# Performance work log

Measured on AMD Instinct MI355X. Metric: run time of the kernel, lower is better.

The kernel has to match this reference:

```python
import jax, jax.numpy as jnp
import numpy as np

DIST = 200.0
BBOX_SP = 24
N_COARSE = 64
N_BOXES = 10
SAMPLES_ALL = N_COARSE + 2 * N_BOXES  # 84
FR_POS = 10
FR_DIR = 4
NSEM = 50
WID = 256
MERGES = [(39, 41), (27, 26), (28, 26), (29, 26), (30, 26), (31, 26), (9, 8), (35, 13)]


def posenc(x, L):
    f = 2.0 ** jnp.arange(L, dtype=x.dtype)
    xb = x[..., None, :] * f[:, None]                      # [..., L, 3]
    enc = jnp.concatenate([jnp.sin(xb), jnp.cos(xb)], -1)  # [..., L, 6]
    return jnp.concatenate([x, enc.reshape(x.shape[:-1] + (-1,))], -1)


def sample_pdf(bins, weights, n):
    # deterministic inverse-CDF sampling (det=True), bins [B,N,M], weights [B,N,M-1]
    pdf = weights / jnp.sum(weights, -1, keepdims=True)
    cdf = jnp.cumsum(pdf, -1)
    cdf = jnp.concatenate([jnp.zeros_like(cdf[..., :1]), cdf], -1)   # [B,N,M]
    B, N, M = cdf.shape
    u = jnp.linspace(0.0, 1.0, n, dtype=bins.dtype)
    cdf_f = cdf.reshape(B * N, M)
    bins_f = bins.reshape(B * N, M)
    u_f = jnp.broadcast_to(u, (B * N, n))
    inds = jax.vmap(lambda c, uu: jnp.searchsorted(c, uu, side='right'))(cdf_f, u_f)
    below = jnp.clip(inds - 1, 0, M - 1)
    above = jnp.clip(inds, 0, M - 1)
    cdf_b = jnp.take_along_axis(cdf_f, below, 1)
    cdf_a = jnp.take_along_axis(cdf_f, above, 1)
    bin_b = jnp.take_along_axis(bins_f, below, 1)
    bin_a = jnp.take_along_axis(bins_f, above, 1)
    denom = jnp.where(cdf_a - cdf_b < 1e-5, 1.0, cdf_a - cdf_b)
    t = (u_f - cdf_b) / denom
    return (bin_b + t * (bin_a - bin_b)).reshape(B, N, n)


def setup_inputs() -> dict:
    key = jax.random.key(0)
    ks = jax.random.split(key, 16)
    B, N = 1, 2048
    rays_o = jax.random.normal(ks[0], (B, N, 3)) * 2.0
    rays_d = jax.random.normal(ks[1], (B, N, 3))
    rays = jnp.concatenate([rays_o, rays_d], -1)
    near = jax.random.uniform(ks[2], (B, N, N_BOXES), minval=5.0, maxval=150.0)
    far = near + jax.random.uniform(ks[3], (B, N, N_BOXES), minval=5.0, maxval=60.0)
    inst = jax.random.randint(ks[4], (B, N, N_BOXES), 0, 20).astype(jnp.float32)
    label = jax.random.randint(ks[5], (B, N, N_BOXES), 1, NSEM).astype(jnp.float32)
    intersection = jnp.stack([near, far, inst, label], -1)  # [B,N,10,4]
    bg_noise = jax.random.uniform(ks[6], (B, N, SAMPLES_ALL))

    def lin(k, fi, fo):
        return jax.random.normal(k, (fi, fo)) / np.sqrt(fi)

    d_x = 3 + 6 * FR_POS  # 63
    d_d = 3 + 6 * FR_DIR  # 27
    params = dict(
        w_in=lin(ks[7], d_x, WID), b_in=jnp.zeros((WID,)),
        w_h=jax.random.normal(ks[8], (6, WID, WID)) / np.sqrt(WID), b_h=jnp.zeros((6, WID)),
        w_skip=lin(ks[9], WID + d_x, WID), b_skip=jnp.zeros((WID,)),
        w_sigma=lin(ks[10], WID, 1), b_sigma=jnp.zeros((1,)),
        w_feat=lin(ks[11], WID, WID), b_feat=jnp.zeros((WID,)),
        w_rgb1=lin(ks[12], WID + d_d, 128), b_rgb1=jnp.zeros((128,)),
        w_rgb2=lin(ks[13], 128, 3), b_rgb2=jnp.zeros((3,)),
        w_sem=lin(ks[14], WID, NSEM), b_sem=jnp.zeros((NSEM,)),
    )
    out = {'rays': rays, 'intersection': intersection, 'bg_noise': bg_noise}
    out.update(params)
    return out


def reference(rays, intersection, bg_noise, w_in, b_in, w_h, b_h, w_skip, b_skip,
              w_sigma, b_sigma, w_feat, b_feat, w_rgb1, b_rgb1, w_rgb2, b_rgb2,
              w_sem, b_sem):
    B, N, _ = rays.shape
    rays_o, rays_d = rays[..., :3], rays[..., 3:6]
    scale = jnp.linalg.norm(rays_d, axis=-1)  # [B,N]

    # --- ray sampling inside boxes + uniform-PDF resampling ---
    near, far = intersection[..., 0], intersection[..., 1]  # [B,N,10]
    t = jnp.linspace(0.0, 1.0, BBOX_SP)
    z_box = near[..., None] + (far - near)[..., None] * t       # [B,N,10,24]
    z_bound = jnp.concatenate([z_box[..., 0] - 1e-5, z_box[..., -1] + 1e-5], axis=2)  # [B,N,20]
    zf = jnp.sort(z_box.reshape(B, N, -1), axis=2)              # [B,N,240]
    z = sample_pdf(zf, jnp.ones_like(zf[..., 1:]), N_COARSE)    # [B,N,64]
    z = jnp.concatenate([z, z_bound], axis=2)                   # [B,N,84]
    z = jnp.where(z < 0.0, DIST + 20.0 * bg_noise, z)
    z = jnp.sort(z, axis=2)

    # --- NeRF MLP on sample points ---
    xyz = (rays_o[:, :, None] + rays_d[:, :, None] * z[..., None] / scale[..., None, None]) / DIST
    dirs = rays_d / scale[..., None]
    x_enc = posenc(xyz, FR_POS)                                 # [B,N,S,63]
    h = jax.nn.relu(x_enc @ w_in + b_in)
    for i in range(3):
        h = jax.nn.relu(h @ w_h[i] + b_h[i])
    h = jax.nn.relu(jnp.concatenate([h, x_enc], -1) @ w_skip + b_skip)
    for i in range(3, 6):
        h = jax.nn.relu(h @ w_h[i] + b_h[i])
    sigma = (h @ w_sigma + b_sigma)[..., 0]                     # [B,N,S]
    sem = h @ w_sem + b_sem                                     # [B,N,S,50]
    feat = h @ w_feat + b_feat
    d_enc = posenc(dirs, FR_DIR)                                # [B,N,27]
    d_enc = jnp.broadcast_to(d_enc[:, :, None, :], feat.shape[:-1] + (d_enc.shape[-1],))
    hr = jax.nn.relu(jnp.concatenate([feat, d_enc], -1) @ w_rgb1 + b_rgb1)
    rgb = hr @ w_rgb2 + b_rgb2                                  # [B,N,S,3]

    # --- semantic one-hot scatter + boundary masks (no-grad region) ---
    zs = jax.lax.stop_gradient(z)
    nearb = intersection[:, :, None, :, 0]                      # [B,N,1,10]
    farb = intersection[:, :, None, :, 1]
    inside = (zs[..., None] > nearb) & (zs[..., None] < farb)   # [B,N,S,10]
    d1 = zs[..., None] - farb
    d2 = nearb - zs[..., None]
    mask_bound = jnp.any(((d1 > 0) & (d1 < 1e-3)) | ((d2 > 0) & (d2 < 1e-3)), axis=-1)
    labels = intersection[..., 3].astype(jnp.int32)             # [B,N,10]
    oh_box = jax.nn.one_hot(labels, NSEM)                       # [B,N,10,50]
    one_hot = jnp.max(inside[..., None].astype(jnp.float32) * oh_box[:, :, None, :, :], axis=3)
    s0 = one_hot.sum(-1)
    mask_bbox = (zs < DIST) & (s0 == 0.0)
    mask_bg = (zs > DIST) & (s0 == 0.0)
    one_hot = one_hot.at[..., 0].set(jnp.where(mask_bbox, 1.0, one_hot[..., 0]))
    one_hot = one_hot.at[..., 23].set(jnp.where(mask_bg, 1.0, one_hot[..., 23]))
    for src, dst in MERGES:  # training-mode class merging (box/car/park/gate)
        one_hot = one_hot.at[..., dst].set(jnp.maximum(one_hot[..., dst], one_hot[..., src]))
        one_hot = one_hot.at[..., src].set(0.0)
    one_hot = jax.lax.stop_gradient(one_hot)

    # zero density outside boxes and at box boundaries
    sigma = jnp.where(mask_bbox | mask_bound, 0.0, sigma)

    # --- volumetric compositing (raw2outputs_semantic_joint) ---
    z_true = z / scale[..., None]
    dists = jnp.concatenate([z_true[..., 1:] - z_true[..., :-1],
                             jnp.full_like(z_true[..., :1], 1e10)], -1) * scale[..., None]
    alpha = 1.0 - jnp.exp(-jax.nn.relu(sigma) * dists)
    trans = jnp.cumprod(jnp.concatenate([jnp.ones_like(alpha[..., :1]),
                                         1.0 - alpha + 1e-10], -1)[..., :-1], -1)
    w = alpha * trans                                           # [B,N,S]
    rgb_map = jnp.einsum('bns,bnsc->bnc', w, jax.nn.sigmoid(rgb))
    depth = jnp.sum(w * z_true, -1)
    acc = jnp.sum(w, -1)
    sem_map = jnp.einsum('bns,bnsc->bnc', w, sem)
    return jnp.concatenate([rgb_map, depth[..., None], acc[..., None], sem_map], -1)  # [B,N,55]
```

## Files before the change

### kernel.cpp

```cpp
#include <hip/hip_runtime.h>

typedef _Float16 half8 __attribute__((ext_vector_type(8)));
typedef float f32x4  __attribute__((ext_vector_type(4)));
typedef float f32x16 __attribute__((ext_vector_type(16)));

#define NRAYS 2048
#define SAMP 84
#define NPTS (NRAYS*SAMP)
#define SEMSTR 52

#define WT0_OFF   0
#define WTH_OFF   16384
#define WTS_OFF   409600
#define WTHD_OFF  491520
#define WTR1_OFF  573440
#define WTR2_OFF  610304
#define WT_TOTAL  614400
#define NBIAS     2512

#define OFF_WT    ((size_t)0)
#define OFF_BIAS  ((size_t)1228800)
#define OFF_Z     (OFF_BIAS + (size_t)NBIAS*4)
#define OFF_SCALE (OFF_Z + (size_t)NPTS*4)
#define OFF_SIGMA (OFF_SCALE + (size_t)NRAYS*4)
#define OFF_RGB   (OFF_SIGMA + (size_t)NPTS*4)
#define OFF_SEM   (OFF_RGB + (size_t)NPTS*12)

__global__ __launch_bounds__(256) void prep_kernel(
    const float* __restrict__ w_in,  const float* __restrict__ w_h,
    const float* __restrict__ w_skip,const float* __restrict__ w_sigma,
    const float* __restrict__ w_feat,const float* __restrict__ w_rgb1,
    const float* __restrict__ w_rgb2,const float* __restrict__ w_sem,
    const float* __restrict__ b_in,  const float* __restrict__ b_h,
    const float* __restrict__ b_skip,const float* __restrict__ b_sigma,
    const float* __restrict__ b_feat,const float* __restrict__ b_rgb1,
    const float* __restrict__ b_rgb2,const float* __restrict__ b_sem,
    _Float16* __restrict__ wt, float* __restrict__ bias)
{
  int idx = blockIdx.x*256 + threadIdx.x;
  if (idx < WT_TOTAL) {
    float v; int n, k, l, h, kt, F, rem;
    if (idx < WTH_OFF) {
      F = idx >> 11; rem = idx & 2047; kt = rem >> 9; int q = rem & 511;
      l = q >> 3; h = q & 7;
      n = F*32 + (l&31); k = kt*16 + ((l>>5)<<3) + h;
      v = (k < 63) ? w_in[k*256 + n] : 0.f;
    } else if (idx < WTS_OFF) {
      int r = idx - WTH_OFF; int i = r >> 16; int rr = r & 65535;
      F = rr >> 13; rem = rr & 8191; kt = rem >> 9; int q = rem & 511;
      l = q >> 3; h = q & 7;
      n = F*32 + (l&31); k = kt*16 + ((l>>5)<<3) + h;
      v = w_h[(i<<16) + (k<<8) + n];
    } else if (idx < WTHD_OFF) {
      int r = idx - WTS_OFF;
      F = r / 10240; rem = r % 10240; kt = rem >> 9; int q = rem & 511;
      l = q >> 3; h = q & 7;
      n = F*32 + (l&31); k = kt*16 + ((l>>5)<<3) + h;
      v = (k < 319) ? w_skip[k*256 + n] : 0.f;
    } else if (idx < WTR1_OFF) {
      int r = idx - WTHD_OFF;
      F = r >> 13; rem = r & 8191; kt = rem >> 9; int q = rem & 511;
      l = q >> 3; h = q & 7;
      n = F*32 + (l&31); k = kt*16 + ((l>>5)<<3) + h;
      v = (n < 256) ? w_feat[(k<<8) + n]
        : (n < 306) ? w_sem[k*50 + (n-256)]
        : (n == 306)? w_sigma[k] : 0.f;
    } else if (idx < WTR2_OFF) {
      int r = idx - WTR1_OFF;
      F = r / 9216; rem = r % 9216; kt = rem >> 9; int q = rem & 511;
      l = q >> 3; h = q & 7;
      n = F*32 + (l&31); k = kt*16 + ((l>>5)<<3) + h;
      v = (k < 283) ? w_rgb1[k*128 + n] : 0.f;
    } else {
      int r = idx - WTR2_OFF;
      kt = r >> 9; int q = r & 511;
      l = q >> 3; h = q & 7;
      n = (l&31); k = kt*16 + ((l>>5)<<3) + h;
      v = (n < 3) ? w_rgb2[k*3 + n] : 0.f;
    }
    wt[idx] = (_Float16)v;
  } else if (idx < WT_TOTAL + NBIAS) {
    int j = idx - WT_TOTAL; float v;
    if (j < 2048) {
      int i = j >> 8, c = j & 255;
      v = (i==0) ? b_in[c] : (i<4) ? b_h[(i-1)*256+c]
        : (i==4) ? b_skip[c] : b_h[(i-2)*256+c];
    } else if (j < 2368) {
      int c = j - 2048;
      v = (c<256) ? b_feat[c] : (c<306) ? b_sem[c-256]
        : (c==306) ? b_sigma[0] : 0.f;
    } else if (j < 2496) v = b_rgb1[j-2368];
    else { int c = j-2496; v = (c<3) ? b_rgb2[c] : 0.f; }
    bias[j] = v;
  }
}

__global__ __launch_bounds__(256) void sample_kernel(
    const float* __restrict__ rays, const float* __restrict__ inter,
    const float* __restrict__ noise, float* __restrict__ zbuf,
    float* __restrict__ scaleb)
{
  __shared__ float sv[240], ss[240], z2[84];
  const int ray = blockIdx.x, t = threadIdx.x;
  const float* bx = inter + (size_t)ray*40;
  if (t < 240) {
    int b = t/24, j = t%24;
    float nr = bx[b*4], fr = bx[b*4+1];
    float tj = (j==23) ? 1.f : (float)j * (1.f/23.f);
    sv[t] = nr + (fr-nr)*tj;
  }
  __syncthreads();
  if (t < 240) {
    float v = sv[t]; int r = 0;
    for (int i = 0; i < 240; ++i) { float vi = sv[i]; r += (vi < v) || (vi == v && i < t); }
    ss[r] = v;
  }
  __syncthreads();
  if (t < 64) {
    float z;
    if (t == 63) z = ss[239];
    else { int num = t*239; int k = num/63; float f = (float)(num - k*63)*(1.f/63.f);
           z = ss[k] + f*(ss[k+1]-ss[k]); }
    z2[t] = z;
  } else if (t < 84) {
    int b = t - 64;
    z2[t] = (b < 10) ? (bx[b*4] - 1e-5f) : (bx[(b-10)*4+1] + 1e-5f);
  }
  __syncthreads();
  if (t < 84) { float z = z2[t]; if (z < 0.f) z = 200.f + 20.f*noise[(size_t)ray*84 + t]; z2[t] = z; }
  __syncthreads();
  if (t < 84) {
    float v = z2[t]; int r = 0;
    for (int i = 0; i < 84; ++i) { float vi = z2[i]; r += (vi < v) || (vi == v && i < t); }
    zbuf[(size_t)ray*84 + r] = v;
  }
  if (t == 0) {
    float dx = rays[ray*6+3], dy = rays[ray*6+4], dz = rays[ray*6+5];
    scaleb[ray] = sqrtf(dx*dx + dy*dy + dz*dz);
  }
}

#define LDS_TOTAL 40960

__device__ __forceinline__ uint32_t laddr(int m, int k) {
  return (uint32_t)(m*640) + (uint32_t)((((k>>3)^(m&7))<<4) + ((k&7)<<1));
}
struct __attribute__((aligned(8))) H4 { _Float16 h[4]; };

__device__ __forceinline__ float xenc_val(int j, float x0, float x1, float x2) {
  if (j >= 63) return 0.f;
  if (j < 3) return j==0?x0:(j==1?x1:x2);
  int q = j-3, lf = q/6, r = q%6, ci = r%3;
  float xc = (ci==0)?x0:((ci==1)?x1:x2);
  float arg = xc * (float)(1<<lf);
  return (r<3) ? sinf(arg) : cosf(arg);
}
__device__ __forceinline__ float denc_val(int c, float u0, float u1, float u2) {
  if (c >= 27) return 0.f;
  if (c < 3) return c==0?u0:(c==1?u1:u2);
  int q = c-3, lf = q/6, r = q%6, ci = r%3;
  float uc = (ci==0)?u0:((ci==1)?u1:u2);
  float arg = uc * (float)(1<<lf);
  return (r<3) ? sinf(arg) : cosf(arg);
}

template<int KT, int NF, int MODE, bool RELU, int XOFF, bool INPLACE>
__device__ __forceinline__ void gemm(uint8_t* smem,
    const _Float16* __restrict__ WT, int fbase, const float* __restrict__ bias0,
    int p0, float* __restrict__ sigmaws, _Float16* __restrict__ semws)
{
  constexpr int MF = 2;
  const int t = threadIdx.x;
  const int l = t & 63, wn = t >> 6;
  const int lr = l & 31, lg = l >> 5;
  constexpr int DW   = (KT <= 3) ? KT : 4;
  constexpr int LEAD = (KT <= 3) ? KT : 3;
  f32x16 acc[NF][MF];
#pragma unroll
  for (int i = 0; i < NF; ++i)
#pragma unroll
    for (int j = 0; j < MF; ++j)
#pragma unroll
      for (int r = 0; r < 16; ++r) acc[i][j][r] = 0.f;
  const _Float16* wb = WT + (size_t)((fbase + wn*NF)*KT)*512 + (size_t)l*8;
  half8 av[DW][NF];
  half8 bv[2][MF];
  auto baddr = [&](int mf, int kt)->uint32_t {
    return laddr(mf*32 + lr, XOFF + kt*16 + lg*8);
  };
#pragma unroll
  for (int d = 0; d < LEAD && d < KT; ++d)
#pragma unroll
    for (int nf = 0; nf < NF; ++nf)
      av[d][nf] = *(const half8*)(wb + (size_t)(nf*KT + d)*512);
#pragma unroll
  for (int mf = 0; mf < MF; ++mf)
    bv[0][mf] = *(const half8*)(smem + baddr(mf, 0));
#pragma unroll
  for (int kt = 0; kt < KT; ++kt) {
    if (kt + 1 < KT) {
#pragma unroll
      for (int mf = 0; mf < MF; ++mf)
        bv[(kt+1)&1][mf] = *(const half8*)(smem + baddr(mf, kt+1));
    }
    if (kt + LEAD < KT) {
#pragma unroll
      for (int nf = 0; nf < NF; ++nf)
        av[(kt+LEAD)%DW][nf] = *(const half8*)(wb + (size_t)(nf*KT + kt + LEAD)*512);
    }
    __builtin_amdgcn_sched_barrier(0);
#pragma unroll
    for (int nf = 0; nf < NF; ++nf)
#pragma unroll
      for (int mf = 0; mf < MF; ++mf)
        acc[nf][mf] = __builtin_amdgcn_mfma_f32_32x32x16_f16(
            av[kt%DW][nf], bv[kt&1][mf], acc[nf][mf], 0, 0, 0);
    __builtin_amdgcn_sched_barrier(0);
  }
  if (INPLACE) __syncthreads();
#pragma unroll
  for (int nf = 0; nf < NF; ++nf) {
    const int ncol0 = (fbase + wn*NF + nf)*32;
#pragma unroll
    for (int mf = 0; mf < MF; ++mf) {
      const int m = mf*32 + lr;
      const f32x16 v = acc[nf][mf];
#pragma unroll
      for (int g = 0; g < 4; ++g) {
        const int nst = ncol0 + 8*g + 4*lg;
        const f32x4 b4 = *(const f32x4*)(bias0 + nst);
        float x0 = v[4*g+0] + b4[0], x1 = v[4*g+1] + b4[1];
        float x2 = v[4*g+2] + b4[2], x3 = v[4*g+3] + b4[3];
        if (RELU) { x0 = fmaxf(x0,0.f); x1 = fmaxf(x1,0.f);
                    x2 = fmaxf(x2,0.f); x3 = fmaxf(x3,0.f); }
        if (MODE == 0) {
          H4 hh; hh.h[0]=(_Float16)x0; hh.h[1]=(_Float16)x1;
                 hh.h[2]=(_Float16)x2; hh.h[3]=(_Float16)x3;
          *(H4*)(smem + laddr(m, nst)) = hh;
        } else {
          const int cb = nst - 256;
          const int pp = p0 + m;
          if (cb <= 44) {
            H4 hh; hh.h[0]=(_Float16)x0; hh.h[1]=(_Float16)x1;
                   hh.h[2]=(_Float16)x2; hh.h[3]=(_Float16)x3;
            *(H4*)(semws + (size_t)pp*SEMSTR + cb) = hh;
          } else if (cb == 48) {
            semws[(size_t)pp*SEMSTR + 48] = (_Float16)x0;
            semws[(size_t)pp*SEMSTR + 49] = (_Float16)x1;
            sigmaws[pp] = x2;
          }
        }
      }
    }
  }
}

__device__ __forceinline__ void gemm_rgb2(uint8_t* smem,
    const _Float16* __restrict__ WT, const float* __restrict__ bias,
    int p0, float* __restrict__ rgbws)
{
  const int t = threadIdx.x;
  const int l = t & 63, w = t >> 6;
  if (w >= 2) return;
  const int lr = l & 31, lg = l >> 5;
  f32x16 acc;
#pragma unroll
  for (int r = 0; r < 16; ++r) acc[r] = 0.f;
  const _Float16* wb = WT + (size_t)l*8;
#pragma unroll
  for (int kt = 0; kt < 8; ++kt) {
    half8 a = *(const half8*)(wb + (size_t)kt*512);
    half8 b = *(const half8*)(smem + laddr(w*32 + lr, kt*16 + lg*8));
    acc = __builtin_amdgcn_mfma_f32_32x32x16_f16(a, b, acc, 0, 0, 0);
  }
  if (lg == 0) {
    const int pp = p0 + w*32 + lr;
#pragma unroll
    for (int r = 0; r < 3; ++r)
      rgbws[(size_t)pp*3 + r] = acc[r] + bias[r];
  }
}

__global__ __launch_bounds__(256,3) void mlp_kernel(
    const float* __restrict__ rays, const float* __restrict__ zbuf,
    const float* __restrict__ scaleb, const _Float16* __restrict__ wt,
    const float* __restrict__ bias, float* __restrict__ sigmaws,
    float* __restrict__ rgbws, _Float16* __restrict__ semws)
{
  extern __shared__ uint8_t smem[];
  const int p0 = blockIdx.x*64;
  const int t = threadIdx.x;
  const int m = t & 63, g = t >> 6;
  const int p = p0 + m;
  const int ray = p / SAMP;
  const float sc = scaleb[ray];
  const float z  = zbuf[p];
  const float ox = rays[ray*6+0], oy = rays[ray*6+1], oz = rays[ray*6+2];
  const float dx = rays[ray*6+3], dy = rays[ray*6+4], dz = rays[ray*6+5];
  const float x0 = (ox + dx*z/sc)/200.f;
  const float x1 = (oy + dy*z/sc)/200.f;
  const float x2 = (oz + dz*z/sc)/200.f;
  const float u0 = dx/sc, u1 = dy/sc, u2 = dz/sc;
  {
    union { _Float16 hv[8]; half8 v; } u8;
#pragma unroll
    for (int hf = 0; hf < 2; ++hf) {
      const int j0 = g*16 + hf*8;
#pragma unroll
      for (int jj = 0; jj < 8; ++jj) u8.hv[jj] = (_Float16)xenc_val(j0+jj, x0, x1, x2);
      *(half8*)(smem + laddr(m, 256 + j0)) = u8.v;
    }
  }
  __syncthreads();
  gemm<4 ,2,0,true ,256,false>(smem, wt+WT0_OFF,         0, bias+0,    p0, sigmaws, semws); __syncthreads();
  gemm<16,2,0,true ,0  ,true >(smem, wt+WTH_OFF+0*65536, 0, bias+256,  p0, sigmaws, semws); __syncthreads();
  gemm<16,2,0,true ,0  ,true >(smem, wt+WTH_OFF+1*65536, 0, bias+512,  p0, sigmaws, semws); __syncthreads();
  gemm<16,2,0,true ,0  ,true >(smem, wt+WTH_OFF+2*65536, 0, bias+768,  p0, sigmaws, semws); __syncthreads();
  gemm<20,2,0,true ,0  ,true >(smem, wt+WTS_OFF,         0, bias+1024, p0, sigmaws, semws);
  {
    union { _Float16 hv[8]; half8 v; } u8;
    const int c0 = g*8;
#pragma unroll
    for (int cc = 0; cc < 8; ++cc) u8.hv[cc] = (_Float16)denc_val(c0+cc, u0, u1, u2);
    *(half8*)(smem + laddr(m, 256 + c0)) = u8.v;
  }
  __syncthreads();
  gemm<16,2,0,true ,0  ,true >(smem, wt+WTH_OFF+3*65536, 0, bias+1280, p0, sigmaws, semws); __syncthreads();
  gemm<16,2,0,true ,0  ,true >(smem, wt+WTH_OFF+4*65536, 0, bias+1536, p0, sigmaws, semws); __syncthreads();
  gemm<16,2,0,true ,0  ,true >(smem, wt+WTH_OFF+5*65536, 0, bias+1792, p0, sigmaws, semws); __syncthreads();
  if ((t >> 6) < 2)
    gemm<16,1,1,false,0 ,false>(smem, wt+WTHD_OFF,        8, bias+2048, p0, sigmaws, semws);
  gemm<16,2,0,false,0  ,true >(smem, wt+WTHD_OFF,        0, bias+2048, p0, sigmaws, semws); __syncthreads();
  gemm<18,1,0,true ,0  ,true >(smem, wt+WTR1_OFF,        0, bias+2368, p0, sigmaws, semws); __syncthreads();
  gemm_rgb2(smem, wt+WTR2_OFF, bias+2496, p0, rgbws);
}

__global__ __launch_bounds__(128) void comp_kernel(
    const float* __restrict__ inter, const float* __restrict__ zbuf,
    const float* __restrict__ scaleb, const float* __restrict__ sigmaws,
    const float* __restrict__ rgbws, const _Float16* __restrict__ semws,
    float* __restrict__ out)
{
  __shared__ float zt[84], alpha[84], wgt[84];
  const int ray = blockIdx.x, t = threadIdx.x;
  const float sc = scaleb[ray];
  const float* bx = inter + (size_t)ray*40;
  if (t < 84) zt[t] = zbuf[(size_t)ray*84 + t] / sc;
  __syncthreads();
  if (t < 84) {
    const float z = zbuf[(size_t)ray*84 + t];
    bool inside = false, bound = false;
    for (int b = 0; b < 10; ++b) {
      const float nr = bx[b*4], fr = bx[b*4+1];
      inside = inside || (z > nr && z < fr);
      const float d1 = z - fr, d2 = nr - z;
      bound = bound || (d1 > 0.f && d1 < 1e-3f) || (d2 > 0.f && d2 < 1e-3f);
    }
    float sg = sigmaws[(size_t)ray*84 + t];
    const bool bbox = (z < 200.f) && !inside;
    if (bbox || bound) sg = 0.f;
    sg = fmaxf(sg, 0.f);
    const float dist = (t < 83) ? (zt[t+1] - zt[t])*sc : 1e10f*sc;
    alpha[t] = 1.f - expf(-sg*dist);
  }
  __syncthreads();
  if (t == 0) {
    float T = 1.f;
    for (int s = 0; s < 84; ++s) { wgt[s] = alpha[s]*T; T *= (1.f - alpha[s] + 1e-10f); }
  }
  __syncthreads();
  if (t < 55) {
    float a = 0.f;
    const size_t base = (size_t)ray*84;
    if (t < 50) {
      for (int s = 0; s < 84; ++s) a += wgt[s]*(float)semws[(base+s)*SEMSTR + t];
      out[(size_t)ray*55 + 5 + t] = a;
    } else if (t < 53) {
      const int c = t - 50;
      for (int s = 0; s < 84; ++s) { const float r = rgbws[(base+s)*3 + c]; a += wgt[s]/(1.f + expf(-r)); }
      out[(size_t)ray*55 + c] = a;
    } else if (t == 53) {
      for (int s = 0; s < 84; ++s) a += wgt[s]*zt[s];
      out[(size_t)ray*55 + 3] = a;
    } else {
      for (int s = 0; s < 84; ++s) a += wgt[s];
      out[(size_t)ray*55 + 4] = a;
    }
  }
}

extern "C" void kernel_launch(void* const* d_in, const int* in_sizes, int n_in,
                              void* d_out, int out_size, void* d_ws, size_t ws_size,
                              hipStream_t stream) {
  const float* rays   = (const float*)d_in[0];
  const float* inter  = (const float*)d_in[1];
  const float* noise  = (const float*)d_in[2];
  const float* w_in   = (const float*)d_in[3];
  const float* b_in   = (const float*)d_in[4];
  const float* w_h    = (const float*)d_in[5];
  const float* b_h    = (const float*)d_in[6];
  const float* w_skip = (const float*)d_in[7];
  const float* b_skip = (const float*)d_in[8];
  const float* w_sig  = (const float*)d_in[9];
  const float* b_sig  = (const float*)d_in[10];
  const float* w_feat = (const float*)d_in[11];
  const float* b_feat = (const float*)d_in[12];
  const float* w_rgb1 = (const float*)d_in[13];
  const float* b_rgb1 = (const float*)d_in[14];
  const float* w_rgb2 = (const float*)d_in[15];
  const float* b_rgb2 = (const float*)d_in[16];
  const float* w_sem  = (const float*)d_in[17];
  const float* b_sem  = (const float*)d_in[18];

  uint8_t* ws = (uint8_t*)d_ws;
  _Float16* wt    = (_Float16*)(ws + OFF_WT);
  float* bias     = (float*)(ws + OFF_BIAS);
  float* zbuf     = (float*)(ws + OFF_Z);
  float* scaleb   = (float*)(ws + OFF_SCALE);
  float* sigmaws  = (float*)(ws + OFF_SIGMA);
  float* rgbws    = (float*)(ws + OFF_RGB);
  _Float16* semws = (_Float16*)(ws + OFF_SEM);

  prep_kernel<<<dim3((WT_TOTAL + NBIAS + 255)/256), dim3(256), 0, stream>>>(
      w_in, w_h, w_skip, w_sig, w_feat, w_rgb1, w_rgb2, w_sem,
      b_in, b_h, b_skip, b_sig, b_feat, b_rgb1, b_rgb2, b_sem, wt, bias);
  sample_kernel<<<dim3(NRAYS), dim3(256), 0, stream>>>(rays, inter, noise, zbuf, scaleb);
  mlp_kernel<<<dim3(NPTS/64), dim3(256), LDS_TOTAL, stream>>>(
      rays, zbuf, scaleb, wt, bias, sigmaws, rgbws, semws);
  comp_kernel<<<dim3(NRAYS), dim3(128), 0, stream>>>(
      inter, zbuf, scaleb, sigmaws, rgbws, semws, (float*)d_out);
}
```

Measured before the change: 292.6 us.

## Double MLP point tile per block and pack bias/ReLU epilogue in fp16

Each MLP block now handles 128 points instead of 64 (MF=4, LDS doubled, grid halved, occupancy hint lowered to 2). This reuses each loaded weight fragment across twice as many MFMAs. The hidden-layer epilogue now converts accumulators to packed fp16 first and does bias add and ReLU in half2, using a new fp16 bias buffer. The trade-offs are more registers and LDS per block, fewer resident blocks, and slightly lower epilogue precision. The early return for waves 2-3 in gemm_rgb2 was also removed, which may change which waves run that stage.

```diff
diff --git a/kernel.cpp b/kernel.cpp
--- a/kernel.cpp
+++ b/kernel.cpp
@@ -1,6 +1,7 @@
 #include <hip/hip_runtime.h>
 
 typedef _Float16 half8 __attribute__((ext_vector_type(8)));
+typedef __fp16  half2v __attribute__((ext_vector_type(2)));
 typedef float f32x4  __attribute__((ext_vector_type(4)));
 typedef float f32x16 __attribute__((ext_vector_type(16)));
 
@@ -20,7 +21,8 @@
 
 #define OFF_WT    ((size_t)0)
 #define OFF_BIAS  ((size_t)1228800)
-#define OFF_Z     (OFF_BIAS + (size_t)NBIAS*4)
+#define OFF_BIASH ((size_t)1238848)
+#define OFF_Z     ((size_t)1243904)
 #define OFF_SCALE (OFF_Z + (size_t)NPTS*4)
 #define OFF_SIGMA (OFF_SCALE + (size_t)NRAYS*4)
 #define OFF_RGB   (OFF_SIGMA + (size_t)NPTS*4)
@@ -35,7 +37,8 @@
     const float* __restrict__ b_skip,const float* __restrict__ b_sigma,
     const float* __restrict__ b_feat,const float* __restrict__ b_rgb1,
     const float* __restrict__ b_rgb2,const float* __restrict__ b_sem,
-    _Float16* __restrict__ wt, float* __restrict__ bias)
+    _Float16* __restrict__ wt, float* __restrict__ bias,
+    _Float16* __restrict__ biasH)
 {
   int idx = blockIdx.x*256 + threadIdx.x;
   if (idx < WT_TOTAL) {
@@ -92,6 +95,7 @@
     } else if (j < 2496) v = b_rgb1[j-2368];
     else { int c = j-2496; v = (c<3) ? b_rgb2[c] : 0.f; }
     bias[j] = v;
+    biasH[j] = (_Float16)v;
   }
 }
 
@@ -140,7 +144,7 @@
   }
 }
 
-#define LDS_TOTAL 40960
+#define LDS_TOTAL 81920
 
 __device__ __forceinline__ uint32_t laddr(int m, int k) {
   return (uint32_t)(m*640) + (uint32_t)((((k>>3)^(m&7))<<4) + ((k&7)<<1));
@@ -166,10 +170,11 @@
 
 template<int KT, int NF, int MODE, bool RELU, int XOFF, bool INPLACE>
 __device__ __forceinline__ void gemm(uint8_t* smem,
-    const _Float16* __restrict__ WT, int fbase, const float* __restrict__ bias0,
+    const _Float16* __restrict__ WT, int fbase,
+    const float* __restrict__ bias0, const _Float16* __restrict__ biasH0,
     int p0, float* __restrict__ sigmaws, _Float16* __restrict__ semws)
 {
-  constexpr int MF = 2;
+  constexpr int MF = 4;
   const int t = threadIdx.x;
   const int l = t & 63, wn = t >> 6;
   const int lr = l & 31, lg = l >> 5;
@@ -228,26 +233,32 @@
 #pragma unroll
       for (int g = 0; g < 4; ++g) {
         const int nst = ncol0 + 8*g + 4*lg;
-        const f32x4 b4 = *(const f32x4*)(bias0 + nst);
-        float x0 = v[4*g+0] + b4[0], x1 = v[4*g+1] + b4[1];
-        float x2 = v[4*g+2] + b4[2], x3 = v[4*g+3] + b4[3];
-        if (RELU) { x0 = fmaxf(x0,0.f); x1 = fmaxf(x1,0.f);
-                    x2 = fmaxf(x2,0.f); x3 = fmaxf(x3,0.f); }
         if (MODE == 0) {
-          H4 hh; hh.h[0]=(_Float16)x0; hh.h[1]=(_Float16)x1;
-                 hh.h[2]=(_Float16)x2; hh.h[3]=(_Float16)x3;
+          half2v h0 = __builtin_amdgcn_cvt_pkrtz(v[4*g+0], v[4*g+1]);
+          half2v h1 = __builtin_amdgcn_cvt_pkrtz(v[4*g+2], v[4*g+3]);
+          const half2v* bh = (const half2v*)(biasH0 + nst);
+          h0 = h0 + bh[0];
+          h1 = h1 + bh[1];
+          if (RELU) {
+            h0 = __builtin_elementwise_max(h0, (half2v)(__fp16)0);
+            h1 = __builtin_elementwise_max(h1, (half2v)(__fp16)0);
+          }
+          H4 hh; *(half2v*)&hh.h[0] = h0; *(half2v*)&hh.h[2] = h1;
           *(H4*)(smem + laddr(m, nst)) = hh;
         } else {
+          const f32x4 b4 = *(const f32x4*)(bias0 + nst);
+          float y0 = v[4*g+0] + b4[0], y1 = v[4*g+1] + b4[1];
+          float y2 = v[4*g+2] + b4[2], y3 = v[4*g+3] + b4[3];
           const int cb = nst - 256;
           const int pp = p0 + m;
           if (cb <= 44) {
-            H4 hh; hh.h[0]=(_Float16)x0; hh.h[1]=(_Float16)x1;
-                   hh.h[2]=(_Float16)x2; hh.h[3]=(_Float16)x3;
+            H4 hh; hh.h[0]=(_Float16)y0; hh.h[1]=(_Float16)y1;
+                   hh.h[2]=(_Float16)y2; hh.h[3]=(_Float16)y3;
             *(H4*)(semws + (size_t)pp*SEMSTR + cb) = hh;
           } else if (cb == 48) {
-            semws[(size_t)pp*SEMSTR + 48] = (_Float16)x0;
-            semws[(size_t)pp*SEMSTR + 49] = (_Float16)x1;
-            sigmaws[pp] = x2;
+            semws[(size_t)pp*SEMSTR + 48] = (_Float16)y0;
+            semws[(size_t)pp*SEMSTR + 49] = (_Float16)y1;
+            sigmaws[pp] = y2;
           }
         }
       }
@@ -261,7 +272,6 @@
 {
   const int t = threadIdx.x;
   const int l = t & 63, w = t >> 6;
-  if (w >= 2) return;
   const int lr = l & 31, lg = l >> 5;
   f32x16 acc;
 #pragma unroll
@@ -281,16 +291,17 @@
   }
 }
 
-__global__ __launch_bounds__(256,3) void mlp_kernel(
+__global__ __launch_bounds__(256,2) void mlp_kernel(
     const float* __restrict__ rays, const float* __restrict__ zbuf,
     const float* __restrict__ scaleb, const _Float16* __restrict__ wt,
-    const float* __restrict__ bias, float* __restrict__ sigmaws,
-    float* __restrict__ rgbws, _Float16* __restrict__ semws)
+    const float* __restrict__ bias, const _Float16* __restrict__ biasH,
+    float* __restrict__ sigmaws, float* __restrict__ rgbws,
+    _Float16* __restrict__ semws)
 {
   extern __shared__ uint8_t smem[];
-  const int p0 = blockIdx.x*64;
+  const int p0 = blockIdx.x*128;
   const int t = threadIdx.x;
-  const int m = t & 63, g = t >> 6;
+  const int m = t & 127, g = t >> 7;
   const int p = p0 + m;
   const int ray = p / SAMP;
   const float sc = scaleb[ray];
@@ -304,34 +315,37 @@
   {
     union { _Float16 hv[8]; half8 v; } u8;
 #pragma unroll
-    for (int hf = 0; hf < 2; ++hf) {
-      const int j0 = g*16 + hf*8;
+    for (int q = 0; q < 4; ++q) {
+      const int j0 = g*32 + q*8;
 #pragma unroll
       for (int jj = 0; jj < 8; ++jj) u8.hv[jj] = (_Float16)xenc_val(j0+jj, x0, x1, x2);
       *(half8*)(smem + laddr(m, 256 + j0)) = u8.v;
     }
   }
   __syncthreads();
-  gemm<4 ,2,0,true ,256,false>(smem, wt+WT0_OFF,         0, bias+0,    p0, sigmaws, semws); __syncthreads();
-  gemm<16,2,0,true ,0  ,true >(smem, wt+WTH_OFF+0*65536, 0, bias+256,  p0, sigmaws, semws); __syncthreads();
-  gemm<16,2,0,true ,0  ,true >(smem, wt+WTH_OFF+1*65536, 0, bias+512,  p0, sigmaws, semws); __syncthreads();
-  gemm<16,2,0,true ,0  ,true >(smem, wt+WTH_OFF+2*65536, 0, bias+768,  p0, sigmaws, semws); __syncthreads();
-  gemm<20,2,0,true ,0  ,true >(smem, wt+WTS_OFF,         0, bias+1024, p0, sigmaws, semws);
+  gemm<4 ,2,0,true ,256,false>(smem, wt+WT0_OFF,         0, bias+0,    biasH+0,    p0, sigmaws, semws); __syncthreads();
+  gemm<16,2,0,true ,0  ,true >(smem, wt+WTH_OFF+0*65536, 0, bias+256,  biasH+256,  p0, sigmaws, semws); __syncthreads();
+  gemm<16,2,0,true ,0  ,true >(smem, wt+WTH_OFF+1*65536, 0, bias+512,  biasH+512,  p0, sigmaws, semws); __syncthreads();
+  gemm<16,2,0,true ,0  ,true >(smem, wt+WTH_OFF+2*65536, 0, bias+768,  biasH+768,  p0, sigmaws, semws); __syncthreads();
+  gemm<20,2,0,true ,0  ,true >(smem, wt+WTS_OFF,         0, bias+1024, biasH+1024, p0, sigmaws, semws);
   {
     union { _Float16 hv[8]; half8 v; } u8;
-    const int c0 = g*8;
-#pragma unroll
-    for (int cc = 0; cc < 8; ++cc) u8.hv[cc] = (_Float16)denc_val(c0+cc, u0, u1, u2);
-    *(half8*)(smem + laddr(m, 256 + c0)) = u8.v;
-  }
-  __syncthreads();
-  gemm<16,2,0,true ,0  ,true >(smem, wt+WTH_OFF+3*65536, 0, bias+1280, p0, sigmaws, semws); __syncthreads();
-  gemm<16,2,0,true ,0  ,true >(smem, wt+WTH_OFF+4*65536, 0, bias+1536, p0, sigmaws, semws); __syncthreads();
-  gemm<16,2,0,true ,0  ,true >(smem, wt+WTH_OFF+5*65536, 0, bias+1792, p0, sigmaws, semws); __syncthreads();
+#pragma unroll
+    for (int hf = 0; hf < 2; ++hf) {
+      const int c0 = g*16 + hf*8;
+#pragma unroll
+      for (int cc = 0; cc < 8; ++cc) u8.hv[cc] = (_Float16)denc_val(c0+cc, u0, u1, u2);
+      *(half8*)(smem + laddr(m, 256 + c0)) = u8.v;
+    }
+  }
+  __syncthreads();
+  gemm<16,2,0,true ,0  ,true >(smem, wt+WTH_OFF+3*65536, 0, bias+1280, biasH+1280, p0, sigmaws, semws); __syncthreads();
+  gemm<16,2,0,true ,0  ,true >(smem, wt+WTH_OFF+4*65536, 0, bias+1536, biasH+1536, p0, sigmaws, semws); __syncthreads();
+  gemm<16,2,0,true ,0  ,true >(smem, wt+WTH_OFF+5*65536, 0, bias+1792, biasH+1792, p0, sigmaws, semws); __syncthreads();
   if ((t >> 6) < 2)
-    gemm<16,1,1,false,0 ,false>(smem, wt+WTHD_OFF,        8, bias+2048, p0, sigmaws, semws);
-  gemm<16,2,0,false,0  ,true >(smem, wt+WTHD_OFF,        0, bias+2048, p0, sigmaws, semws); __syncthreads();
-  gemm<18,1,0,true ,0  ,true >(smem, wt+WTR1_OFF,        0, bias+2368, p0, sigmaws, semws); __syncthreads();
+    gemm<16,1,1,false,0 ,false>(smem, wt+WTHD_OFF,        8, bias+2048, biasH+2048, p0, sigmaws, semws);
+  gemm<16,2,0,false,0  ,true >(smem, wt+WTHD_OFF,        0, bias+2048, biasH+2048, p0, sigmaws, semws); __syncthreads();
+  gemm<18,1,0,true ,0  ,true >(smem, wt+WTR1_OFF,        0, bias+2368, biasH+2368, p0, sigmaws, semws); __syncthreads();
   gemm_rgb2(smem, wt+WTR2_OFF, bias+2496, p0, rgbws);
 }
 
@@ -415,6 +429,7 @@
   uint8_t* ws = (uint8_t*)d_ws;
   _Float16* wt    = (_Float16*)(ws + OFF_WT);
   float* bias     = (float*)(ws + OFF_BIAS);
+  _Float16* biasH = (_Float16*)(ws + OFF_BIASH);
   float* zbuf     = (float*)(ws + OFF_Z);
   float* scaleb   = (float*)(ws + OFF_SCALE);
   float* sigmaws  = (float*)(ws + OFF_SIGMA);
@@ -423,10 +438,10 @@
 
   prep_kernel<<<dim3((WT_TOTAL + NBIAS + 255)/256), dim3(256), 0, stream>>>(
       w_in, w_h, w_skip, w_sig, w_feat, w_rgb1, w_rgb2, w_sem,
-      b_in, b_h, b_skip, b_sig, b_feat, b_rgb1, b_rgb2, b_sem, wt, bias);
+      b_in, b_h, b_skip, b_sig, b_feat, b_rgb1, b_rgb2, b_sem, wt, bias, biasH);
   sample_kernel<<<dim3(NRAYS), dim3(256), 0, stream>>>(rays, inter, noise, zbuf, scaleb);
-  mlp_kernel<<<dim3(NPTS/64), dim3(256), LDS_TOTAL, stream>>>(
-      rays, zbuf, scaleb, wt, bias, sigmaws, rgbws, semws);
+  mlp_kernel<<<dim3(NPTS/128), dim3(256), LDS_TOTAL, stream>>>(
+      rays, zbuf, scaleb, wt, bias, biasH, sigmaws, rgbws, semws);
   comp_kernel<<<dim3(NRAYS), dim3(128), 0, stream>>>(
       inter, zbuf, scaleb, sigmaws, rgbws, semws, (float*)d_out);
 }
```

New measurement: 279.0 us. 4.6% less time.
